# Optimization experiments

Measured on AMD Instinct MI355X. Metric: run time of the kernel, lower is better.

The kernel has to match this reference:

```python
import jax, jax.numpy as jnp
import numpy as np
import math

EMBED_DIM = 2048
NUM_HEADS = 32
NUM_KV_HEADS = 8
HEAD_DIM = EMBED_DIM // NUM_HEADS  # 64
N_REP = NUM_HEADS // NUM_KV_HEADS  # 4
BATCH = 2
SEQ = 2048


def _rope_tables(seq_len, head_dim):
    # standard RoPE tables matching rotate_half convention (frequencies tiled twice)
    inv_freq = 1.0 / (10000.0 ** (np.arange(0, head_dim, 2, dtype=np.float32) / head_dim))
    t = np.arange(seq_len, dtype=np.float32)
    freqs = np.outer(t, inv_freq)                      # (seq, head_dim/2)
    emb = np.concatenate([freqs, freqs], axis=-1)      # (seq, head_dim)
    return jnp.asarray(np.cos(emb)), jnp.asarray(np.sin(emb))


def setup_inputs() -> dict:
    key = jax.random.key(0)
    ks = jax.random.split(key, 6)
    scale = 1.0 / math.sqrt(EMBED_DIM)
    x = jax.random.normal(ks[0], (BATCH, SEQ, EMBED_DIM), dtype=jnp.float32)
    wq = jax.random.normal(ks[1], (EMBED_DIM, EMBED_DIM), dtype=jnp.float32) * scale
    wk = jax.random.normal(ks[2], (NUM_KV_HEADS * HEAD_DIM, EMBED_DIM), dtype=jnp.float32) * scale
    wv = jax.random.normal(ks[3], (NUM_KV_HEADS * HEAD_DIM, EMBED_DIM), dtype=jnp.float32) * scale
    wo = jax.random.normal(ks[4], (EMBED_DIM, EMBED_DIM), dtype=jnp.float32) * scale
    freqs_cos, freqs_sin = _rope_tables(SEQ, HEAD_DIM)
    return {"x": x, "freqs_cos": freqs_cos, "freqs_sin": freqs_sin,
            "wq": wq, "wk": wk, "wv": wv, "wo": wo}


def _rotate_half(t):
    h = t.shape[-1] // 2
    return jnp.concatenate([-t[..., h:], t[..., :h]], axis=-1)


def reference(x, freqs_cos, freqs_sin, wq, wk, wv, wo):
    b, s, _ = x.shape
    # QKV projections (Linear with weight (out,in): y = x @ W^T)
    xq = (x @ wq.T).reshape(b, s, NUM_HEADS, HEAD_DIM).transpose(0, 2, 1, 3)     # (b,H,s,d)
    xk = (x @ wk.T).reshape(b, s, NUM_KV_HEADS, HEAD_DIM).transpose(0, 2, 1, 3)  # (b,Hkv,s,d)
    xv = (x @ wv.T).reshape(b, s, NUM_KV_HEADS, HEAD_DIM).transpose(0, 2, 1, 3)
    # RoPE: cos/sin (s,d) broadcast over (b,h,s,d)
    xq = xq * freqs_cos + _rotate_half(xq) * freqs_sin
    xk = xk * freqs_cos + _rotate_half(xk) * freqs_sin
    # GQA: repeat_interleave kv heads to match q heads
    xk = jnp.repeat(xk, N_REP, axis=1)  # (b,H,s,d)
    xv = jnp.repeat(xv, N_REP, axis=1)
    scores = jnp.einsum('bhqd,bhkd->bhqk', xq, xk) / math.sqrt(HEAD_DIM)
    causal = jnp.tril(jnp.ones((s, s), dtype=bool))
    scores = jnp.where(causal, scores, jnp.float32(-1e30))
    attn = jax.nn.softmax(scores, axis=-1)
    out = jnp.einsum('bhqk,bhkd->bhqd', attn, xv)        # (b,H,s,d)
    out = out.transpose(0, 2, 1, 3).reshape(b, s, EMBED_DIM)
    return out @ wo.T
```

## Files before the change

kernel.cpp:

```cpp
#include <hip/hip_runtime.h>

#define BATCH 2
#define SEQ 2048
#define EMBED 2048
#define NHEADS 32
#define NKV 8
#define HDIM 64
#define QKV_LD 3072
#define LOG2E 1.44269504088896f

typedef __attribute__((ext_vector_type(8))) short short8;
typedef __attribute__((ext_vector_type(4))) float f32x4;

__device__ inline float hw_exp2(float x) { return __builtin_amdgcn_exp2f(x); }

__device__ inline ushort f2bf(float f) {
  union { float f; unsigned u; } v{f};
  unsigned r = v.u + 0x7FFF + ((v.u >> 16) & 1);
  return (ushort)(r >> 16);
}
__device__ inline float bf2f(ushort u) {
  union { unsigned u; float f; } v{((unsigned)u) << 16};
  return v.f;
}
__device__ inline unsigned fbits(float f) {
  union { float f; unsigned u; } v{f};
  return v.u;
}

__device__ inline void gload16(const ushort* g, ushort* l) {
  __builtin_amdgcn_global_load_lds(
      (const __attribute__((address_space(1))) unsigned*)g,
      (__attribute__((address_space(3))) unsigned*)l, 16, 0, 0);
}

__global__ __launch_bounds__(256) void cvt_all(const float* __restrict__ x,
                                               const float* __restrict__ wq,
                                               const float* __restrict__ wk,
                                               const float* __restrict__ wv,
                                               const float* __restrict__ wo,
                                               ushort* __restrict__ xb,
                                               ushort* __restrict__ wqkv,
                                               ushort* __restrict__ wob) {
  size_t e = (size_t)(blockIdx.x * blockDim.x + threadIdx.x) * 8;
  const float* src;
  ushort* dst;
  if (e < 8388608u) { src = x + e; dst = xb + e; }
  else if (e < 12582912u) { size_t o = e - 8388608u; src = wq + o; dst = wqkv + o; }
  else if (e < 13631488u) { size_t o = e - 12582912u; src = wk + o; dst = wqkv + 4194304u + o; }
  else if (e < 14680064u) { size_t o = e - 13631488u; src = wv + o; dst = wqkv + 5242880u + o; }
  else { size_t o = e - 14680064u; src = wo + o; dst = wob + o; }
  float4 v0 = ((const float4*)src)[0];
  float4 v1 = ((const float4*)src)[1];
  union { uint4 v; ushort u[8]; } pk;
  pk.u[0] = f2bf(v0.x); pk.u[1] = f2bf(v0.y); pk.u[2] = f2bf(v0.z); pk.u[3] = f2bf(v0.w);
  pk.u[4] = f2bf(v1.x); pk.u[5] = f2bf(v1.y); pk.u[6] = f2bf(v1.z); pk.u[7] = f2bf(v1.w);
  *(uint4*)dst = pk.v;
}

template <typename OutT>
__global__ __launch_bounds__(256) void gemm_bf16(const ushort* __restrict__ A,
                                                 const ushort* __restrict__ B,
                                                 OutT* __restrict__ C,
                                                 int M, int N, int K) {
  __shared__ ushort As[128][32];
  __shared__ ushort Bs[128][32];
  const int tid = threadIdx.x;
  const int lane = tid & 63, wave = tid >> 6;
  const int quad = lane >> 4, l16 = lane & 15;
  const int m0 = blockIdx.y * 128, n0 = blockIdx.x * 128;
  const int wm = (wave >> 1) * 64, wn = (wave & 1) * 64;
  const int srow = lane >> 2, skq = (lane & 3) * 8;

  f32x4 acc[4][4] = {};
  for (int k0 = 0; k0 < K; k0 += 32) {
    const ushort* ga = A + (size_t)(m0 + wave * 32 + srow) * K + k0 + skq;
    const ushort* gb = B + (size_t)(n0 + wave * 32 + srow) * K + k0 + skq;
    __syncthreads();
    gload16(ga, &As[wave * 32][0]);
    gload16(ga + (size_t)16 * K, &As[wave * 32 + 16][0]);
    gload16(gb, &Bs[wave * 32][0]);
    gload16(gb + (size_t)16 * K, &Bs[wave * 32 + 16][0]);
    __syncthreads();
    short8 af[4], bf[4];
#pragma unroll
    for (int i = 0; i < 4; i++) af[i] = *(short8*)&As[wm + i * 16 + l16][quad * 8];
#pragma unroll
    for (int j = 0; j < 4; j++) bf[j] = *(short8*)&Bs[wn + j * 16 + l16][quad * 8];
#pragma unroll
    for (int i = 0; i < 4; i++)
#pragma unroll
      for (int j = 0; j < 4; j++)
        acc[i][j] = __builtin_amdgcn_mfma_f32_16x16x32_bf16(af[i], bf[j], acc[i][j], 0, 0, 0);
  }
#pragma unroll
  for (int i = 0; i < 4; i++) {
#pragma unroll
    for (int r = 0; r < 4; r++) {
      size_t rg = (size_t)(m0 + wm + i * 16 + quad * 4 + r);
#pragma unroll
      for (int j = 0; j < 4; j++) {
        float v = acc[i][j][r];
        int cg = n0 + wn + j * 16 + l16;
        if constexpr (sizeof(OutT) == 2)
          C[rg * N + cg] = f2bf(v);
        else
          C[rg * N + cg] = v;
      }
    }
  }
}

__global__ __launch_bounds__(256) void rope_qk(ushort* __restrict__ t,
                                               const float* __restrict__ fc,
                                               const float* __restrict__ fs,
                                               int total) {
  int idx = blockIdx.x * blockDim.x + threadIdx.x;
  if (idx >= total) return;
  int g = idx & 3;
  int hh = (idx >> 2) % 40;
  int tok = idx / 160;
  int s = tok & (SEQ - 1);
  float scale = (hh < 32) ? 0.125f * LOG2E : 1.0f;
  ushort* p = t + (size_t)tok * QKV_LD + hh * 64 + g * 8;
  union { uint4 v; ushort u[8]; } lo, hi, olo, ohi;
  lo.v = *(const uint4*)p;
  hi.v = *(const uint4*)(p + 32);
  const float* fcb = fc + s * HDIM + g * 8;
  const float* fsb = fs + s * HDIM + g * 8;
  float4 c0a = ((const float4*)fcb)[0], c0b = ((const float4*)fcb)[1];
  float4 s0a = ((const float4*)fsb)[0], s0b = ((const float4*)fsb)[1];
  float4 c1a = ((const float4*)(fcb + 32))[0], c1b = ((const float4*)(fcb + 32))[1];
  float4 s1a = ((const float4*)(fsb + 32))[0], s1b = ((const float4*)(fsb + 32))[1];
  float cc0[8] = {c0a.x, c0a.y, c0a.z, c0a.w, c0b.x, c0b.y, c0b.z, c0b.w};
  float ss0[8] = {s0a.x, s0a.y, s0a.z, s0a.w, s0b.x, s0b.y, s0b.z, s0b.w};
  float cc1[8] = {c1a.x, c1a.y, c1a.z, c1a.w, c1b.x, c1b.y, c1b.z, c1b.w};
  float ss1[8] = {s1a.x, s1a.y, s1a.z, s1a.w, s1b.x, s1b.y, s1b.z, s1b.w};
#pragma unroll
  for (int j = 0; j < 8; j++) {
    float x0 = bf2f(lo.u[j]), x1 = bf2f(hi.u[j]);
    olo.u[j] = f2bf((x0 * cc0[j] - x1 * ss0[j]) * scale);
    ohi.u[j] = f2bf((x1 * cc1[j] + x0 * ss1[j]) * scale);
  }
  *(uint4*)p = olo.v;
  *(uint4*)(p + 32) = ohi.v;
}

__global__ __launch_bounds__(256) void attn_mfma(const ushort* __restrict__ QKV,
                                                 ushort* __restrict__ O) {
  __shared__ ushort Ks[64][72];
  __shared__ ushort Vt[64][72];
  __shared__ ushort Pw[4][16][72];
  const int tid = threadIdx.x;
  const int lane = tid & 63, wave = tid >> 6;
  const int quad = lane >> 4, l16 = lane & 15;
  const int bh = blockIdx.y;
  const int b = bh >> 5, h = bh & 31, kh = h >> 2;
  const int p = blockIdx.x;
  const int qt[2] = {p, 31 - p};
  const int ntiles = 32 - p;

  short8 qf[2][2];
#pragma unroll
  for (int u = 0; u < 2; u++)
#pragma unroll
    for (int c = 0; c < 2; c++)
      qf[u][c] = *(const short8*)(QKV +
          (size_t)(b * SEQ + qt[u] * 64 + wave * 16 + l16) * QKV_LD +
          h * HDIM + c * 32 + quad * 8);

  f32x4 o[2][4] = {};
  float m[2] = {-INFINITY, -INFINITY}, l[2] = {0.f, 0.f};

  const ushort* Kbase = QKV + (size_t)b * SEQ * QKV_LD + 2048 + kh * HDIM;
  const ushort* Vbase = Kbase + 512;
  const int kp = tid & 31, dg = tid >> 5;
  const int relrow = wave * 16 + l16;

  for (int t = 0; t < ntiles; t++) {
    const int k0 = t * 64;
    __syncthreads();
    {
      const float4* kpp = (const float4*)(Kbase + (size_t)(k0 + lane) * QKV_LD + wave * 16);
      float4 kv0 = kpp[0], kv1 = kpp[1];
      const uint4* va4 = (const uint4*)(Vbase + (size_t)(k0 + 2 * kp) * QKV_LD + dg * 8);
      const uint4* vb4 = (const uint4*)(Vbase + (size_t)(k0 + 2 * kp + 1) * QKV_LD + dg * 8);
      uint4 va = va4[0], vb = vb4[0];
      *(float4*)&Ks[lane][wave * 16] = kv0;
      *(float4*)&Ks[lane][wave * 16 + 8] = kv1;
      const unsigned* vaw = (const unsigned*)&va;
      const unsigned* vbw = (const unsigned*)&vb;
#pragma unroll
      for (int j = 0; j < 8; j++) {
        unsigned pk = (j & 1)
            ? __builtin_amdgcn_perm(vbw[j >> 1], vaw[j >> 1], 0x07060302)
            : __builtin_amdgcn_perm(vbw[j >> 1], vaw[j >> 1], 0x05040100);
        *(unsigned*)&Vt[dg * 8 + j][2 * kp] = pk;
      }
    }
    __syncthreads();

#pragma unroll
    for (int u = 0; u < 2; u++) {
      const int diag = qt[u];
      if (t > diag) continue;

      f32x4 s[4];
#pragma unroll
      for (int nt = 0; nt < 4; nt++) {
        short8 kf0 = *(short8*)&Ks[nt * 16 + l16][quad * 8];
        short8 kf1 = *(short8*)&Ks[nt * 16 + l16][32 + quad * 8];
        f32x4 z = {};
        z = __builtin_amdgcn_mfma_f32_16x16x32_bf16(kf0, qf[u][0], z, 0, 0, 0);
        s[nt] = __builtin_amdgcn_mfma_f32_16x16x32_bf16(kf1, qf[u][1], z, 0, 0, 0);
      }

      if (t == diag) {
#pragma unroll
        for (int nt = 0; nt < 4; nt++)
#pragma unroll
          for (int r = 0; r < 4; r++)
            if (nt * 16 + quad * 4 + r > relrow) s[nt][r] = -INFINITY;
      }

      float mx = -INFINITY;
#pragma unroll
      for (int nt = 0; nt < 4; nt++)
#pragma unroll
        for (int r = 0; r < 4; r++) mx = fmaxf(mx, s[nt][r]);
      mx = fmaxf(mx, __shfl_xor(mx, 16));
      mx = fmaxf(mx, __shfl_xor(mx, 32));
      float mnew = fmaxf(m[u], mx);
      float al = hw_exp2(m[u] - mnew);
      m[u] = mnew;

      float pv[16];
      float psum = 0.f;
#pragma unroll
      for (int nt = 0; nt < 4; nt++)
#pragma unroll
        for (int r = 0; r < 4; r++) {
          float pe = hw_exp2(s[nt][r] - mnew);
          pv[nt * 4 + r] = pe;
          psum += pe;
        }
      psum += __shfl_xor(psum, 16);
      psum += __shfl_xor(psum, 32);
      l[u] = l[u] * al + psum;
#pragma unroll
      for (int dt = 0; dt < 4; dt++)
#pragma unroll
        for (int r = 0; r < 4; r++) o[u][dt][r] *= al;

#pragma unroll
      for (int nt = 0; nt < 4; nt++) {
        unsigned lo = __builtin_amdgcn_perm(fbits(pv[nt * 4 + 1]), fbits(pv[nt * 4 + 0]), 0x07060302);
        unsigned hi = __builtin_amdgcn_perm(fbits(pv[nt * 4 + 3]), fbits(pv[nt * 4 + 2]), 0x07060302);
        uint2 pk; pk.x = lo; pk.y = hi;
        *(uint2*)&Pw[wave][l16][nt * 16 + quad * 4] = pk;
      }
      short8 pf0 = *(short8*)&Pw[wave][l16][quad * 8];
      short8 pf1 = *(short8*)&Pw[wave][l16][32 + quad * 8];
#pragma unroll
      for (int dt = 0; dt < 4; dt++) {
        short8 vf0 = *(short8*)&Vt[dt * 16 + l16][quad * 8];
        short8 vf1 = *(short8*)&Vt[dt * 16 + l16][32 + quad * 8];
        o[u][dt] = __builtin_amdgcn_mfma_f32_16x16x32_bf16(vf0, pf0, o[u][dt], 0, 0, 0);
        o[u][dt] = __builtin_amdgcn_mfma_f32_16x16x32_bf16(vf1, pf1, o[u][dt], 0, 0, 0);
      }
    }
  }

#pragma unroll
  for (int u = 0; u < 2; u++) {
    float inv = 1.0f / l[u];
    size_t rowg = (size_t)(b * SEQ + qt[u] * 64 + wave * 16 + l16) * EMBED + h * HDIM;
#pragma unroll
    for (int dt = 0; dt < 4; dt++) {
      ushort q0 = f2bf(o[u][dt][0] * inv), q1 = f2bf(o[u][dt][1] * inv);
      ushort q2 = f2bf(o[u][dt][2] * inv), q3 = f2bf(o[u][dt][3] * inv);
      uint2 pk;
      pk.x = (unsigned)q0 | ((unsigned)q1 << 16);
      pk.y = (unsigned)q2 | ((unsigned)q3 << 16);
      *(uint2*)&O[rowg + dt * 16 + quad * 4] = pk;
    }
  }
}

extern "C" void kernel_launch(void* const* d_in, const int* in_sizes, int n_in,
                              void* d_out, int out_size, void* d_ws, size_t ws_size,
                              hipStream_t stream) {
  const float* x = (const float*)d_in[0];
  const float* fcos = (const float*)d_in[1];
  const float* fsin = (const float*)d_in[2];
  const float* wq = (const float*)d_in[3];
  const float* wk = (const float*)d_in[4];
  const float* wv = (const float*)d_in[5];
  const float* wo = (const float*)d_in[6];
  float* out = (float*)d_out;

  const int M = BATCH * SEQ;
  ushort* ws = (ushort*)d_ws;
  ushort* xb = ws;
  ushort* wqkv = xb + (size_t)M * EMBED;
  ushort* wob = wqkv + (size_t)QKV_LD * EMBED;
  ushort* QKVb = wob + (size_t)EMBED * EMBED;
  ushort* Ab = QKVb + (size_t)M * QKV_LD;

  dim3 blk(256);
  cvt_all<<<9216, blk, 0, stream>>>(x, wq, wk, wv, wo, xb, wqkv, wob);

  gemm_bf16<ushort><<<dim3(QKV_LD / 128, M / 128), blk, 0, stream>>>(xb, wqkv, QKVb, M, QKV_LD, EMBED);

  {
    int tot = M * 40 * 4;
    rope_qk<<<(tot + 255) / 256, blk, 0, stream>>>(QKVb, fcos, fsin, tot);
  }

  attn_mfma<<<dim3(16, BATCH * NHEADS), blk, 0, stream>>>(QKVb, Ab);

  gemm_bf16<float><<<dim3(EMBED / 128, M / 128), blk, 0, stream>>>(Ab, wob, out, M, EMBED, EMBED);
}
```

Before: 328.2 us.

## Fuse RoPE into QKV GEMM epilogue and hoist K/V fragments in attention

Applies RoPE and the Q scaling inside the QKV GEMM epilogue, which removes the separate rope kernel and its full read-modify-write pass over Q/K. In attention, the K and V fragments are loaded from LDS once per tile and shared by both query tiles instead of being reloaded for each, the Vt row is padded to change its bank mapping, and the rescale of the accumulator is skipped when the running max is unchanged across the whole wavefront. These changes add register pressure and a wave-uniform branch in exchange for less LDS traffic and one fewer launch.

```diff
diff --git a/kernel.cpp b/kernel.cpp
--- a/kernel.cpp
+++ b/kernel.cpp
@@ -58,11 +58,13 @@
   *(uint4*)dst = pk.v;
 }
 
-template <typename OutT>
+template <typename OutT, bool DoRope>
 __global__ __launch_bounds__(256) void gemm_bf16(const ushort* __restrict__ A,
                                                  const ushort* __restrict__ B,
                                                  OutT* __restrict__ C,
-                                                 int M, int N, int K) {
+                                                 int M, int N, int K,
+                                                 const float* __restrict__ fc,
+                                                 const float* __restrict__ fs) {
   __shared__ ushort As[128][32];
   __shared__ ushort Bs[128][32];
   const int tid = threadIdx.x;
@@ -93,6 +95,31 @@
       for (int j = 0; j < 4; j++)
         acc[i][j] = __builtin_amdgcn_mfma_f32_16x16x32_bf16(af[i], bf[j], acc[i][j], 0, 0, 0);
   }
+
+  if constexpr (DoRope) {
+    const int hd = (n0 + wn) >> 6;
+    if (hd < 40) {
+      const float scale = (hd < 32) ? 0.125f * LOG2E : 1.0f;
+#pragma unroll
+      for (int i = 0; i < 4; i++) {
+#pragma unroll
+        for (int r = 0; r < 4; r++) {
+          int s = (m0 + wm + i * 16 + quad * 4 + r) & (SEQ - 1);
+          const float* fcb = fc + s * HDIM + l16;
+          const float* fsb = fs + s * HDIM + l16;
+          float c0 = fcb[0], c1 = fcb[16], c2 = fcb[32], c3 = fcb[48];
+          float s0 = fsb[0], s1 = fsb[16], s2 = fsb[32], s3 = fsb[48];
+          float x0 = acc[i][0][r], x1 = acc[i][1][r];
+          float x2 = acc[i][2][r], x3 = acc[i][3][r];
+          acc[i][0][r] = (x0 * c0 - x2 * s0) * scale;
+          acc[i][1][r] = (x1 * c1 - x3 * s1) * scale;
+          acc[i][2][r] = (x2 * c2 + x0 * s2) * scale;
+          acc[i][3][r] = (x3 * c3 + x1 * s3) * scale;
+        }
+      }
+    }
+  }
+
 #pragma unroll
   for (int i = 0; i < 4; i++) {
 #pragma unroll
@@ -111,45 +138,10 @@
   }
 }
 
-__global__ __launch_bounds__(256) void rope_qk(ushort* __restrict__ t,
-                                               const float* __restrict__ fc,
-                                               const float* __restrict__ fs,
-                                               int total) {
-  int idx = blockIdx.x * blockDim.x + threadIdx.x;
-  if (idx >= total) return;
-  int g = idx & 3;
-  int hh = (idx >> 2) % 40;
-  int tok = idx / 160;
-  int s = tok & (SEQ - 1);
-  float scale = (hh < 32) ? 0.125f * LOG2E : 1.0f;
-  ushort* p = t + (size_t)tok * QKV_LD + hh * 64 + g * 8;
-  union { uint4 v; ushort u[8]; } lo, hi, olo, ohi;
-  lo.v = *(const uint4*)p;
-  hi.v = *(const uint4*)(p + 32);
-  const float* fcb = fc + s * HDIM + g * 8;
-  const float* fsb = fs + s * HDIM + g * 8;
-  float4 c0a = ((const float4*)fcb)[0], c0b = ((const float4*)fcb)[1];
-  float4 s0a = ((const float4*)fsb)[0], s0b = ((const float4*)fsb)[1];
-  float4 c1a = ((const float4*)(fcb + 32))[0], c1b = ((const float4*)(fcb + 32))[1];
-  float4 s1a = ((const float4*)(fsb + 32))[0], s1b = ((const float4*)(fsb + 32))[1];
-  float cc0[8] = {c0a.x, c0a.y, c0a.z, c0a.w, c0b.x, c0b.y, c0b.z, c0b.w};
-  float ss0[8] = {s0a.x, s0a.y, s0a.z, s0a.w, s0b.x, s0b.y, s0b.z, s0b.w};
-  float cc1[8] = {c1a.x, c1a.y, c1a.z, c1a.w, c1b.x, c1b.y, c1b.z, c1b.w};
-  float ss1[8] = {s1a.x, s1a.y, s1a.z, s1a.w, s1b.x, s1b.y, s1b.z, s1b.w};
-#pragma unroll
-  for (int j = 0; j < 8; j++) {
-    float x0 = bf2f(lo.u[j]), x1 = bf2f(hi.u[j]);
-    olo.u[j] = f2bf((x0 * cc0[j] - x1 * ss0[j]) * scale);
-    ohi.u[j] = f2bf((x1 * cc1[j] + x0 * ss1[j]) * scale);
-  }
-  *(uint4*)p = olo.v;
-  *(uint4*)(p + 32) = ohi.v;
-}
-
 __global__ __launch_bounds__(256) void attn_mfma(const ushort* __restrict__ QKV,
                                                  ushort* __restrict__ O) {
   __shared__ ushort Ks[64][72];
-  __shared__ ushort Vt[64][72];
+  __shared__ ushort Vt[64][76];
   __shared__ ushort Pw[4][16][72];
   const int tid = threadIdx.x;
   const int lane = tid & 63, wave = tid >> 6;
@@ -200,6 +192,18 @@
     }
     __syncthreads();
 
+    short8 kf[4][2], vf[4][2];
+#pragma unroll
+    for (int nt = 0; nt < 4; nt++) {
+      kf[nt][0] = *(short8*)&Ks[nt * 16 + l16][quad * 8];
+      kf[nt][1] = *(short8*)&Ks[nt * 16 + l16][32 + quad * 8];
+    }
+#pragma unroll
+    for (int dt = 0; dt < 4; dt++) {
+      vf[dt][0] = *(short8*)&Vt[dt * 16 + l16][quad * 8];
+      vf[dt][1] = *(short8*)&Vt[dt * 16 + l16][32 + quad * 8];
+    }
+
 #pragma unroll
     for (int u = 0; u < 2; u++) {
       const int diag = qt[u];
@@ -208,11 +212,9 @@
       f32x4 s[4];
 #pragma unroll
       for (int nt = 0; nt < 4; nt++) {
-        short8 kf0 = *(short8*)&Ks[nt * 16 + l16][quad * 8];
-        short8 kf1 = *(short8*)&Ks[nt * 16 + l16][32 + quad * 8];
         f32x4 z = {};
-        z = __builtin_amdgcn_mfma_f32_16x16x32_bf16(kf0, qf[u][0], z, 0, 0, 0);
-        s[nt] = __builtin_amdgcn_mfma_f32_16x16x32_bf16(kf1, qf[u][1], z, 0, 0, 0);
+        z = __builtin_amdgcn_mfma_f32_16x16x32_bf16(kf[nt][0], qf[u][0], z, 0, 0, 0);
+        s[nt] = __builtin_amdgcn_mfma_f32_16x16x32_bf16(kf[nt][1], qf[u][1], z, 0, 0, 0);
       }
 
       if (t == diag) {
@@ -231,8 +233,16 @@
       mx = fmaxf(mx, __shfl_xor(mx, 16));
       mx = fmaxf(mx, __shfl_xor(mx, 32));
       float mnew = fmaxf(m[u], mx);
-      float al = hw_exp2(m[u] - mnew);
-      m[u] = mnew;
+
+      if (!__all(mnew == m[u])) {
+        float al = hw_exp2(m[u] - mnew);
+        l[u] *= al;
+#pragma unroll
+        for (int dt = 0; dt < 4; dt++)
+#pragma unroll
+          for (int r = 0; r < 4; r++) o[u][dt][r] *= al;
+        m[u] = mnew;
+      }
 
       float pv[16];
       float psum = 0.f;
@@ -240,17 +250,13 @@
       for (int nt = 0; nt < 4; nt++)
 #pragma unroll
         for (int r = 0; r < 4; r++) {
-          float pe = hw_exp2(s[nt][r] - mnew);
+          float pe = hw_exp2(s[nt][r] - m[u]);
           pv[nt * 4 + r] = pe;
           psum += pe;
         }
       psum += __shfl_xor(psum, 16);
       psum += __shfl_xor(psum, 32);
-      l[u] = l[u] * al + psum;
-#pragma unroll
-      for (int dt = 0; dt < 4; dt++)
-#pragma unroll
-        for (int r = 0; r < 4; r++) o[u][dt][r] *= al;
+      l[u] += psum;
 
 #pragma unroll
       for (int nt = 0; nt < 4; nt++) {
@@ -263,10 +269,8 @@
       short8 pf1 = *(short8*)&Pw[wave][l16][32 + quad * 8];
 #pragma unroll
       for (int dt = 0; dt < 4; dt++) {
-        short8 vf0 = *(short8*)&Vt[dt * 16 + l16][quad * 8];
-        short8 vf1 = *(short8*)&Vt[dt * 16 + l16][32 + quad * 8];
-        o[u][dt] = __builtin_amdgcn_mfma_f32_16x16x32_bf16(vf0, pf0, o[u][dt], 0, 0, 0);
-        o[u][dt] = __builtin_amdgcn_mfma_f32_16x16x32_bf16(vf1, pf1, o[u][dt], 0, 0, 0);
+        o[u][dt] = __builtin_amdgcn_mfma_f32_16x16x32_bf16(vf[dt][0], pf0, o[u][dt], 0, 0, 0);
+        o[u][dt] = __builtin_amdgcn_mfma_f32_16x16x32_bf16(vf[dt][1], pf1, o[u][dt], 0, 0, 0);
       }
     }
   }
@@ -310,14 +314,11 @@
   dim3 blk(256);
   cvt_all<<<9216, blk, 0, stream>>>(x, wq, wk, wv, wo, xb, wqkv, wob);
 
-  gemm_bf16<ushort><<<dim3(QKV_LD / 128, M / 128), blk, 0, stream>>>(xb, wqkv, QKVb, M, QKV_LD, EMBED);
-
-  {
-    int tot = M * 40 * 4;
-    rope_qk<<<(tot + 255) / 256, blk, 0, stream>>>(QKVb, fcos, fsin, tot);
-  }
+  gemm_bf16<ushort, true><<<dim3(QKV_LD / 128, M / 128), blk, 0, stream>>>(
+      xb, wqkv, QKVb, M, QKV_LD, EMBED, fcos, fsin);
 
   attn_mfma<<<dim3(16, BATCH * NHEADS), blk, 0, stream>>>(QKVb, Ab);
 
-  gemm_bf16<float><<<dim3(EMBED / 128, M / 128), blk, 0, stream>>>(Ab, wob, out, M, EMBED, EMBED);
-}
+  gemm_bf16<float, false><<<dim3(EMBED / 128, M / 128), blk, 0, stream>>>(
+      Ab, wob, out, M, EMBED, EMBED, nullptr, nullptr);
+}
```

New measurement: 391.6 us. +19.3%, slower.
